# Performance work log

Measured on AMD Instinct MI355X. Metric: run time of the kernel, lower is better.

Reference implementation:

```python
import jax, jax.numpy as jnp
import numpy as np

N = 100000      # num nodes
E = 1000000     # num edges
R = 50          # num relations
B = 2           # num bases (hard-coded in source)
IN, HID, OUT = 128, 64, 64


def setup_inputs() -> dict:
    key = jax.random.key(0)
    ks = jax.random.split(key, 12)
    def xavier(k, shape):
        fan_in, fan_out = shape[-2], shape[-1]
        lim = (6.0 / (fan_in + fan_out)) ** 0.5
        return jax.random.uniform(k, shape, jnp.float32, -lim, lim)
    return {
        "node_emb": xavier(ks[0], (N, IN)),
        "basis1": xavier(ks[1], (B, IN, HID)),
        "comp1": xavier(ks[2], (R, B)),
        "loop_w1": xavier(ks[3], (IN, HID)),
        "bias1": jnp.zeros((HID,), jnp.float32),
        "basis2": xavier(ks[4], (B, HID, OUT)),
        "comp2": xavier(ks[5], (R, B)),
        "loop_w2": xavier(ks[6], (HID, OUT)),
        "bias2": jnp.zeros((OUT,), jnp.float32),
        "src": jax.random.randint(ks[7], (E,), 0, N, jnp.int32),
        "dst": jax.random.randint(ks[8], (E,), 0, N, jnp.int32),
        "etypes": jax.random.randint(ks[9], (E,), 0, R, jnp.int32),
    }


def _rel_graph_conv(h, basis, comp, loop_w, bias, src, dst, etypes, act):
    # Basis-decomposed R-GCN layer (DGL RelGraphConv, regularizer='basis'):
    #   W_r = sum_b comp[r,b] * basis[b];  m_e = W_{etype_e} h_{src_e}
    # Low-rank form: project with each basis first (2 dense GEMMs), then mix
    # per-edge with the relation coefficients, then scatter-add by dst.
    hb = jnp.einsum('nd,bdo->nbo', h, basis)          # [N, B, out]
    c = comp[etypes]                                   # [E, B]
    msg = jnp.einsum('eb,ebo->eo', c, hb[src])         # gather [E,B,out] -> [E,out]
    agg = jax.ops.segment_sum(msg, dst, num_segments=h.shape[0])  # scatter-add
    return act(agg + h @ loop_w + bias)                # self-loop + bias + activation


def reference(node_emb, basis1, comp1, loop_w1, bias1,
              basis2, comp2, loop_w2, bias2, src, dst, etypes):
    h = _rel_graph_conv(node_emb, basis1, comp1, loop_w1, bias1,
                        src, dst, etypes, jnp.tanh)
    out = _rel_graph_conv(h, basis2, comp2, loop_w2, bias2,
                          src, dst, etypes, jax.nn.relu)
    return out
```

## Files before the change

### kernel.cpp

```cpp
#include <hip/hip_runtime.h>
#include <math.h>


typedef short          short8 __attribute__((ext_vector_type(8)));
typedef float          f32x4  __attribute__((ext_vector_type(4)));
typedef unsigned short u16;

#define NCHUNK 256

static __device__ __forceinline__ u16 bf16_rne(float x) {
    unsigned u = __float_as_uint(x);
    return (u16)((u + 0x7fffu + ((u >> 16) & 1u)) >> 16);
}
static __device__ __forceinline__ float bf16_f32(u16 h) {
    return __uint_as_float(((unsigned)h) << 16);
}

#define DOT2_ACC(acc, vv, cc) \
    asm("v_dot2_f32_bf16 %0, %1, %2, %0" : "+v"(acc) : "v"(vv), "s"(cc))

__device__ __forceinline__ void wconv_body(
    int tid,
    const float* __restrict__ loopw1, const float* __restrict__ basis1,
    const float* __restrict__ loopw2, const float* __restrict__ basis2,
    const float* __restrict__ comp1, const float* __restrict__ comp2,
    u16* __restrict__ wt1h, u16* __restrict__ wt1l,
    u16* __restrict__ wt2h, u16* __restrict__ wt2l,
    unsigned* __restrict__ cpk1, unsigned* __restrict__ cpk2)
{
    if (tid < 192 * 128) {
        const int j = tid >> 7, k = tid & 127;
        const float w = (j < 64)
            ? loopw1[k * 64 + j]
            : basis1[(size_t)((j - 64) >> 6) * (128 * 64) + k * 64 + ((j - 64) & 63)];
        const u16 h = bf16_rne(w);
        wt1h[tid] = h;
        wt1l[tid] = bf16_rne(w - bf16_f32(h));
    }
    if (tid < 192 * 64) {
        const int j = tid >> 6, k = tid & 63;
        const float w = (j < 64)
            ? loopw2[k * 64 + j]
            : basis2[(size_t)((j - 64) >> 6) * (64 * 64) + k * 64 + ((j - 64) & 63)];
        const u16 h = bf16_rne(w);
        wt2h[tid] = h;
        wt2l[tid] = bf16_rne(w - bf16_f32(h));
    }
    if (tid < 50) {
        cpk1[tid] = (unsigned)bf16_rne(comp1[2 * tid])
                  | ((unsigned)bf16_rne(comp1[2 * tid + 1]) << 16);
        cpk2[tid] = (unsigned)bf16_rne(comp2[2 * tid])
                  | ((unsigned)bf16_rne(comp2[2 * tid + 1]) << 16);
    }
}

__global__ __launch_bounds__(256) void prep_count(
    const int* __restrict__ dst, int* __restrict__ cnt, int nE, int nB,
    const float* __restrict__ loopw1, const float* __restrict__ basis1,
    const float* __restrict__ loopw2, const float* __restrict__ basis2,
    const float* __restrict__ comp1, const float* __restrict__ comp2,
    u16* __restrict__ wt1h, u16* __restrict__ wt1l,
    u16* __restrict__ wt2h, u16* __restrict__ wt2l,
    unsigned* __restrict__ cpk1, unsigned* __restrict__ cpk2)
{
    const int t = threadIdx.x;
    if (blockIdx.x >= NCHUNK) {
        wconv_body((blockIdx.x - NCHUNK) * 256 + t,
                   loopw1, basis1, loopw2, basis2, comp1, comp2,
                   wt1h, wt1l, wt2h, wt2l, cpk1, cpk2);
        return;
    }
    __shared__ int lh[1024];
    for (int b = t; b < 1024; b += 256) lh[b] = 0;
    __syncthreads();
    const int chunk = (nE + NCHUNK - 1) / NCHUNK;
    const int e0 = blockIdx.x * chunk;
    const int e1 = min(nE, e0 + chunk);
    for (int e = e0 + t; e < e1; e += 256)
        atomicAdd(&lh[dst[e] >> 7], 1);
    __syncthreads();
    for (int b = t; b < nB; b += 256)
        cnt[blockIdx.x * nB + b] = lh[b];
}

template<int K>
__global__ __launch_bounds__(512, 2) void rgcn_dense_mfma(
    const float* __restrict__ x,
    const u16* __restrict__ wth,
    const u16* __restrict__ wtl,
    const float* __restrict__ bias,
    float* __restrict__ self,
    unsigned* __restrict__ hbb,
    int nNodes)
{
    constexpr int KC    = K / 32;
    constexpr int GW    = K / 8;
    constexpr int GMW   = GW - 1;
    constexpr int CCOLS = (K == 128) ? 48 : 192;
    constexpr int NCH   = 192 / CCOLS;
    constexpr int JH    = CCOLS / 16;
    constexpr int TG    = CCOLS * 2 * GW;
    constexpr int PG    = TG / 512;
    constexpr int BUF   = CCOLS * 2 * K;
    __shared__ u16 wlds[24576];

    const int n0   = blockIdx.x * 128;
    const int lane = threadIdx.x & 63;
    const int w    = threadIdx.x >> 6;
    const int rl   = lane & 15;
    const int kb   = lane >> 4;

    const int row = n0 + w * 16 + rl;
    short8 Ah[KC], Al[KC];
    #pragma unroll
    for (int kc = 0; kc < KC; ++kc) {
        float v[8];
        if (row < nNodes) {
            const float* xp = x + (size_t)row * K + kc * 32 + kb * 8;
            const float4 a = *reinterpret_cast<const float4*>(xp);
            const float4 b = *reinterpret_cast<const float4*>(xp + 4);
            v[0] = a.x; v[1] = a.y; v[2] = a.z; v[3] = a.w;
            v[4] = b.x; v[5] = b.y; v[6] = b.z; v[7] = b.w;
        } else {
            #pragma unroll
            for (int i = 0; i < 8; ++i) v[i] = 0.f;
        }
        #pragma unroll
        for (int i = 0; i < 8; ++i) {
            const u16 h = bf16_rne(v[i]);
            Ah[kc][i] = (short)h;
            Al[kc][i] = (short)bf16_rne(v[i] - bf16_f32(h));
        }
    }

    f32x4 acc[12];
    #pragma unroll
    for (int j = 0; j < 12; ++j) acc[j] = (f32x4){0.f, 0.f, 0.f, 0.f};

    auto load_chunk = [&](int cc, short8* sreg) {
        #pragma unroll
        for (int i = 0; i < PG; ++i) {
            const int gi = (int)threadIdx.x + i * 512;
            const int ch = gi / (2 * GW);
            const int r2 = gi - ch * 2 * GW;
            const int s  = r2 / GW;
            const int g  = r2 - s * GW;
            sreg[i] = *reinterpret_cast<const short8*>(
                (s == 0 ? wth : wtl) + (size_t)(cc * CCOLS + ch) * K + g * 8);
        }
    };
    auto write_chunk = [&](u16* buf, const short8* sreg) {
        #pragma unroll
        for (int i = 0; i < PG; ++i) {
            const int gi = (int)threadIdx.x + i * 512;
            const int ch = gi / (2 * GW);
            const int r2 = gi - ch * 2 * GW;
            const int s  = r2 / GW;
            const int g  = r2 - s * GW;
            *reinterpret_cast<short8*>(
                &buf[((ch * 2 + s) * GW + (g ^ (ch & GMW))) * 8]) = sreg[i];
        }
    };
    auto compute = [&](int cc, const u16* buf) {
        #pragma unroll
        for (int j16h = 0; j16h < JH; ++j16h) {
            const int ch = j16h * 16 + rl;
            const u16* bbase = &buf[(ch * 2) * GW * 8];
            #pragma unroll
            for (int kc = 0; kc < KC; ++kc) {
                const int gp = (kc * 4 + kb) ^ (ch & GMW);
                const short8 Bh =
                    *reinterpret_cast<const short8*>(bbase + gp * 8);
                const short8 Bl =
                    *reinterpret_cast<const short8*>(bbase + (GW + gp) * 8);
                f32x4 a = acc[cc * JH + j16h];
                a = __builtin_amdgcn_mfma_f32_16x16x32_bf16(Ah[kc], Bh, a, 0, 0, 0);
                a = __builtin_amdgcn_mfma_f32_16x16x32_bf16(Ah[kc], Bl, a, 0, 0, 0);
                a = __builtin_amdgcn_mfma_f32_16x16x32_bf16(Al[kc], Bh, a, 0, 0, 0);
                acc[cc * JH + j16h] = a;
            }
        }
    };

    if constexpr (NCH == 1) {
        short8 s0[PG];
        load_chunk(0, s0);
        write_chunk(wlds, s0);
        __syncthreads();
        compute(0, wlds);
    } else {
        short8 s0[PG];
        load_chunk(0, s0);
        write_chunk(wlds, s0);
        __syncthreads();
        #pragma unroll
        for (int cc = 0; cc < 4; ++cc) {
            short8 sn[PG];
            if (cc < 3) load_chunk(cc + 1, sn);
            compute(cc, &wlds[(cc & 1) * BUF]);
            __syncthreads();
            if (cc < 3) {
                write_chunk(&wlds[((cc + 1) & 1) * BUF], sn);
                __syncthreads();
            }
        }
    }

    const int rowbase = n0 + w * 16 + kb * 4;
    #pragma unroll
    for (int j16 = 0; j16 < 4; ++j16) {
        const float bj = bias[j16 * 16 + rl];
        #pragma unroll
        for (int r = 0; r < 4; ++r) {
            const int rr = rowbase + r;
            if (rr < nNodes)
                self[(size_t)rr * 64 + j16 * 16 + rl] = acc[j16][r] + bj;
        }
    }
    #pragma unroll
    for (int j16 = 4; j16 < 8; ++j16) {
        #pragma unroll
        for (int r = 0; r < 4; ++r) {
            const int rr = rowbase + r;
            if (rr < nNodes)
                hbb[(size_t)rr * 64 + (j16 - 4) * 16 + rl] =
                    (unsigned)bf16_rne(acc[j16][r])
                  | ((unsigned)bf16_rne(acc[j16 + 4][r]) << 16);
        }
    }
}

__global__ __launch_bounds__(NCHUNK) void bkt_chunkscan(
    int* __restrict__ cnt, int* __restrict__ tot, int nB)
{
    __shared__ int sm[NCHUNK];
    const int b = blockIdx.x, t = threadIdx.x;
    const int v = cnt[t * nB + b];
    sm[t] = v;
    __syncthreads();
    for (int off = 1; off < NCHUNK; off <<= 1) {
        const int u = (t >= off) ? sm[t - off] : 0;
        __syncthreads();
        sm[t] += u;
        __syncthreads();
    }
    cnt[t * nB + b] = sm[t] - v;
    if (t == NCHUNK - 1) tot[b] = sm[t];
}

__global__ __launch_bounds__(1024) void bkt_boff(
    const int* __restrict__ tot, int* __restrict__ boff, int nB, int nE)
{
    __shared__ int sm[1024];
    const int t = threadIdx.x;
    const int v = (t < nB) ? tot[t] : 0;
    sm[t] = v; __syncthreads();
    for (int off = 1; off < 1024; off <<= 1) {
        const int u = (t >= off) ? sm[t - off] : 0;
        __syncthreads();
        sm[t] += u;
        __syncthreads();
    }
    if (t < nB) boff[t] = sm[t] - v;
    if (t == 0) boff[nB] = nE;
}

__global__ __launch_bounds__(256) void bkt_scatter(
    const int* __restrict__ src, const int* __restrict__ dst,
    const int* __restrict__ et, const int* __restrict__ cnt,
    const int* __restrict__ boff, unsigned* __restrict__ rec,
    int nE, int nB)
{
    __shared__ int lcur[1024];
    const int t = threadIdx.x;
    const int c = blockIdx.x;
    for (int b = t; b < nB; b += 256)
        lcur[b] = boff[b] + cnt[c * nB + b];
    __syncthreads();
    const int chunk = (nE + NCHUNK - 1) / NCHUNK;
    const int e0 = c * chunk;
    const int e1 = min(nE, e0 + chunk);
    for (int e = e0 + t; e < e1; e += 256) {
        const int d = dst[e];
        const int p = atomicAdd(&lcur[d >> 7], 1);
        rec[p] = ((unsigned)(d & 127) << 23)
               | ((unsigned)src[e] << 6)
               | (unsigned)et[e];
    }
}

__global__ __launch_bounds__(256) void bkt_sort(
    const unsigned* __restrict__ rec, unsigned* __restrict__ rec2,
    const int* __restrict__ boff, int* __restrict__ rowptr,
    int nNodes)
{
    __shared__ int cnt[128];
    __shared__ int pos[128];
    const int b = blockIdx.x;
    const int t = threadIdx.x;
    const int beg = boff[b], end = boff[b + 1];
    if (t < 128) cnt[t] = 0;
    __syncthreads();
    for (int i = beg + t; i < end; i += 256)
        atomicAdd(&cnt[rec[i] >> 23], 1);
    __syncthreads();
    if (t < 128) pos[t] = cnt[t];
    __syncthreads();
    for (int off = 1; off < 128; off <<= 1) {
        int u = 0;
        if (t < 128 && t >= off) u = pos[t - off];
        __syncthreads();
        if (t < 128) pos[t] += u;
        __syncthreads();
    }
    if (t < 128) {
        const int ex = beg + pos[t] - cnt[t];
        pos[t] = ex;
        const int n = (b << 7) + t;
        if (n < nNodes) rowptr[n] = ex;
    }
    __syncthreads();
    for (int i = beg + t; i < end; i += 256) {
        const unsigned r = rec[i];
        const int p = atomicAdd(&pos[r >> 23], 1);
        rec2[p] = r;
    }
}

template<int ACT>
__global__ __launch_bounds__(256) void rgcn_agg(
    const unsigned* __restrict__ hbb,
    const unsigned* __restrict__ cpk,
    const int* __restrict__ rowptr,
    const unsigned* __restrict__ rec2,
    float* __restrict__ io,
    int nNodes, int nEdges)
{
    const int lane = threadIdx.x & 63;
    const int w  = (blockIdx.x * 256 + threadIdx.x) >> 6;
    const int nW = (gridDim.x * 256) >> 6;
    for (int n = w; n < nNodes; n += nW) {
        const int beg = rowptr[n];
        const int end = (n == nNodes - 1) ? nEdges : rowptr[n + 1];
        const float self = io[(size_t)n * 64 + lane];
        float acc0 = 0.f, acc1 = 0.f;
        for (int base = beg; base < end; base += 64) {
            const int cnt = min(64, end - base);
            const unsigned r = (lane < cnt) ? rec2[base + lane] : 0u;
            int i = 0;
            for (; i + 8 <= cnt; i += 8) {
                int ss[8]; unsigned cp[8];
                #pragma unroll
                for (int k = 0; k < 8; ++k) {
                    const unsigned rk =
                        (unsigned)__builtin_amdgcn_readlane((int)r, i + k);
                    ss[k] = (int)((rk >> 6) & 0x1FFFFu);
                    cp[k] = cpk[rk & 63u];
                }
                unsigned v[8];
                #pragma unroll
                for (int k = 0; k < 8; ++k)
                    v[k] = hbb[(size_t)ss[k] * 64 + lane];
                #pragma unroll
                for (int k = 0; k < 8; ++k) {
                    if (k & 1) { DOT2_ACC(acc1, v[k], cp[k]); }
                    else       { DOT2_ACC(acc0, v[k], cp[k]); }
                }
            }
            for (; i + 2 <= cnt; i += 2) {
                const unsigned rA =
                    (unsigned)__builtin_amdgcn_readlane((int)r, i);
                const unsigned rB =
                    (unsigned)__builtin_amdgcn_readlane((int)r, i + 1);
                const unsigned cA = cpk[rA & 63u], cB = cpk[rB & 63u];
                const unsigned vA = hbb[(size_t)((rA >> 6) & 0x1FFFFu) * 64 + lane];
                const unsigned vB = hbb[(size_t)((rB >> 6) & 0x1FFFFu) * 64 + lane];
                DOT2_ACC(acc0, vA, cA);
                DOT2_ACC(acc1, vB, cB);
            }
            if (i < cnt) {
                const unsigned rA =
                    (unsigned)__builtin_amdgcn_readlane((int)r, i);
                const unsigned cA = cpk[rA & 63u];
                const unsigned vA = hbb[(size_t)((rA >> 6) & 0x1FFFFu) * 64 + lane];
                DOT2_ACC(acc0, vA, cA);
            }
        }
        float o = self + acc0 + acc1;
        o = (ACT == 0) ? tanhf(o) : fmaxf(o, 0.f);
        io[(size_t)n * 64 + lane] = o;
    }
}

extern "C" void kernel_launch(void* const* d_in, const int* in_sizes, int n_in,
                              void* d_out, int out_size, void* d_ws, size_t ws_size,
                              hipStream_t stream)
{
    const float* node_emb = (const float*)d_in[0];
    const float* basis1   = (const float*)d_in[1];
    const float* comp1    = (const float*)d_in[2];
    const float* loop_w1  = (const float*)d_in[3];
    const float* bias1    = (const float*)d_in[4];
    const float* basis2   = (const float*)d_in[5];
    const float* comp2    = (const float*)d_in[6];
    const float* loop_w2  = (const float*)d_in[7];
    const float* bias2    = (const float*)d_in[8];
    const int*   src      = (const int*)d_in[9];
    const int*   dst      = (const int*)d_in[10];
    const int*   et       = (const int*)d_in[11];

    const int N = in_sizes[0] / 128;
    const int E = in_sizes[9];
    const int nB = (N + 127) / 128;

    float* out = (float*)d_out;

    unsigned* hbb    = (unsigned*)d_ws;
    float*    h      = (float*)(hbb + (size_t)N * 64);
    unsigned* rec    = (unsigned*)(h + (size_t)N * 64);
    unsigned* rec2   = rec + E;
    int*      cnt    = (int*)(rec2 + E);
    int*      tot    = cnt + NCHUNK * nB;
    int*      boff   = tot + nB;
    int*      rowptr = boff + nB + 1;
    u16*      wt1h   = (u16*)(rowptr + N);
    u16*      wt1l   = wt1h + 192 * 128;
    u16*      wt2h   = wt1l + 192 * 128;
    u16*      wt2l   = wt2h + 192 * 64;
    unsigned* cpk1   = (unsigned*)(wt2l + 192 * 64);
    unsigned* cpk2   = cpk1 + 64;

    const int nBlkDense = (N + 127) / 128;
    const int nBlkAgg   = (N + 3) / 4;

    prep_count<<<NCHUNK + 96, 256, 0, stream>>>(
        dst, cnt, E, nB, loop_w1, basis1, loop_w2, basis2, comp1, comp2,
        wt1h, wt1l, wt2h, wt2l, cpk1, cpk2);

    bkt_chunkscan<<<nB, NCHUNK, 0, stream>>>(cnt, tot, nB);
    bkt_boff     <<<1,    1024, 0, stream>>>(tot, boff, nB, E);
    bkt_scatter  <<<NCHUNK, 256, 0, stream>>>(src, dst, et, cnt, boff, rec, E, nB);
    bkt_sort     <<<nB,     256, 0, stream>>>(rec, rec2, boff, rowptr, N);

    rgcn_dense_mfma<128><<<nBlkDense, 512, 0, stream>>>(
        node_emb, wt1h, wt1l, bias1, h, hbb, N);
    rgcn_agg<0><<<nBlkAgg, 256, 0, stream>>>(
        hbb, cpk1, rowptr, rec2, h, N, E);

    rgcn_dense_mfma<64><<<nBlkDense, 512, 0, stream>>>(
        h, wt2h, wt2l, bias2, out, hbb, N);
    rgcn_agg<1><<<nBlkAgg, 256, 0, stream>>>(
        hbb, cpk2, rowptr, rec2, out, N, E);
}
```

Baseline: 191.0 us.

## Make dense MFMA kernel persistent with resident weights and prefetched A tiles

The dense projection kernel now loads the full 192-column split-bf16 weight matrix into LDS once per block and loops persistently over 128-row node tiles. A fixed grid of 256 or 512 blocks replaces one block per tile. Each iteration prefetches the next tile's activations into registers while the current tile computes. This removes the repeated per-tile weight staging and the chunked double-buffering syncs. In exchange it uses more LDS (96KB for K=128), which may cut occupancy to one block per CU, and adds register pressure from the prefetch buffers.

```diff
diff --git a/kernel.cpp b/kernel.cpp
--- a/kernel.cpp
+++ b/kernel.cpp
@@ -93,79 +93,70 @@
     unsigned* __restrict__ hbb,
     int nNodes)
 {
-    constexpr int KC    = K / 32;
-    constexpr int GW    = K / 8;
-    constexpr int GMW   = GW - 1;
-    constexpr int CCOLS = (K == 128) ? 48 : 192;
-    constexpr int NCH   = 192 / CCOLS;
-    constexpr int JH    = CCOLS / 16;
-    constexpr int TG    = CCOLS * 2 * GW;
-    constexpr int PG    = TG / 512;
-    constexpr int BUF   = CCOLS * 2 * K;
-    __shared__ u16 wlds[24576];
-
-    const int n0   = blockIdx.x * 128;
+    constexpr int KC  = K / 32;
+    constexpr int GW  = K / 8;
+    constexpr int GMW = GW - 1;
+    __shared__ u16 wlds[192 * 2 * K];
+
     const int lane = threadIdx.x & 63;
     const int w    = threadIdx.x >> 6;
     const int rl   = lane & 15;
     const int kb   = lane >> 4;
 
-    const int row = n0 + w * 16 + rl;
-    short8 Ah[KC], Al[KC];
-    #pragma unroll
-    for (int kc = 0; kc < KC; ++kc) {
-        float v[8];
-        if (row < nNodes) {
-            const float* xp = x + (size_t)row * K + kc * 32 + kb * 8;
-            const float4 a = *reinterpret_cast<const float4*>(xp);
-            const float4 b = *reinterpret_cast<const float4*>(xp + 4);
-            v[0] = a.x; v[1] = a.y; v[2] = a.z; v[3] = a.w;
-            v[4] = b.x; v[5] = b.y; v[6] = b.z; v[7] = b.w;
-        } else {
+    for (int gi = threadIdx.x; gi < 192 * 2 * GW; gi += 512) {
+        const int ch = gi / (2 * GW);
+        const int r2 = gi - ch * 2 * GW;
+        const int s  = r2 / GW;
+        const int g  = r2 - s * GW;
+        const short8 vv = *reinterpret_cast<const short8*>(
+            (s == 0 ? wth : wtl) + (size_t)ch * K + g * 8);
+        *reinterpret_cast<short8*>(
+            &wlds[((ch * 2 + s) * GW + (g ^ (ch & GMW))) * 8]) = vv;
+    }
+    __syncthreads();
+
+    const int nT = (nNodes + 127) >> 7;
+
+    auto loadA = [&](int tile, short8* AhD, short8* AlD) {
+        const int row = (tile << 7) + w * 16 + rl;
+        #pragma unroll
+        for (int kc = 0; kc < KC; ++kc) {
+            float v[8];
+            if (row < nNodes) {
+                const float* xp = x + (size_t)row * K + kc * 32 + kb * 8;
+                const float4 a = *reinterpret_cast<const float4*>(xp);
+                const float4 b = *reinterpret_cast<const float4*>(xp + 4);
+                v[0] = a.x; v[1] = a.y; v[2] = a.z; v[3] = a.w;
+                v[4] = b.x; v[5] = b.y; v[6] = b.z; v[7] = b.w;
+            } else {
+                #pragma unroll
+                for (int i = 0; i < 8; ++i) v[i] = 0.f;
+            }
             #pragma unroll
-            for (int i = 0; i < 8; ++i) v[i] = 0.f;
-        }
+            for (int i = 0; i < 8; ++i) {
+                const u16 h = bf16_rne(v[i]);
+                AhD[kc][i] = (short)h;
+                AlD[kc][i] = (short)bf16_rne(v[i] - bf16_f32(h));
+            }
+        }
+    };
+
+    short8 Ah[KC], Al[KC], Ph[KC], Pl[KC];
+    int tile = blockIdx.x;
+    if (tile < nT) loadA(tile, Ah, Al);
+
+    for (; tile < nT; tile += gridDim.x) {
+        const int nxt = tile + gridDim.x;
+        if (nxt < nT) loadA(nxt, Ph, Pl);
+
+        f32x4 acc[12];
         #pragma unroll
-        for (int i = 0; i < 8; ++i) {
-            const u16 h = bf16_rne(v[i]);
-            Ah[kc][i] = (short)h;
-            Al[kc][i] = (short)bf16_rne(v[i] - bf16_f32(h));
-        }
-    }
-
-    f32x4 acc[12];
-    #pragma unroll
-    for (int j = 0; j < 12; ++j) acc[j] = (f32x4){0.f, 0.f, 0.f, 0.f};
-
-    auto load_chunk = [&](int cc, short8* sreg) {
+        for (int j = 0; j < 12; ++j) acc[j] = (f32x4){0.f, 0.f, 0.f, 0.f};
+
         #pragma unroll
-        for (int i = 0; i < PG; ++i) {
-            const int gi = (int)threadIdx.x + i * 512;
-            const int ch = gi / (2 * GW);
-            const int r2 = gi - ch * 2 * GW;
-            const int s  = r2 / GW;
-            const int g  = r2 - s * GW;
-            sreg[i] = *reinterpret_cast<const short8*>(
-                (s == 0 ? wth : wtl) + (size_t)(cc * CCOLS + ch) * K + g * 8);
-        }
-    };
-    auto write_chunk = [&](u16* buf, const short8* sreg) {
-        #pragma unroll
-        for (int i = 0; i < PG; ++i) {
-            const int gi = (int)threadIdx.x + i * 512;
-            const int ch = gi / (2 * GW);
-            const int r2 = gi - ch * 2 * GW;
-            const int s  = r2 / GW;
-            const int g  = r2 - s * GW;
-            *reinterpret_cast<short8*>(
-                &buf[((ch * 2 + s) * GW + (g ^ (ch & GMW))) * 8]) = sreg[i];
-        }
-    };
-    auto compute = [&](int cc, const u16* buf) {
-        #pragma unroll
-        for (int j16h = 0; j16h < JH; ++j16h) {
+        for (int j16h = 0; j16h < 12; ++j16h) {
             const int ch = j16h * 16 + rl;
-            const u16* bbase = &buf[(ch * 2) * GW * 8];
+            const u16* bbase = &wlds[(ch * 2) * GW * 8];
             #pragma unroll
             for (int kc = 0; kc < KC; ++kc) {
                 const int gp = (kc * 4 + kb) ^ (ch & GMW);
@@ -173,59 +164,40 @@
                     *reinterpret_cast<const short8*>(bbase + gp * 8);
                 const short8 Bl =
                     *reinterpret_cast<const short8*>(bbase + (GW + gp) * 8);
-                f32x4 a = acc[cc * JH + j16h];
+                f32x4 a = acc[j16h];
                 a = __builtin_amdgcn_mfma_f32_16x16x32_bf16(Ah[kc], Bh, a, 0, 0, 0);
                 a = __builtin_amdgcn_mfma_f32_16x16x32_bf16(Ah[kc], Bl, a, 0, 0, 0);
                 a = __builtin_amdgcn_mfma_f32_16x16x32_bf16(Al[kc], Bh, a, 0, 0, 0);
-                acc[cc * JH + j16h] = a;
-            }
-        }
-    };
-
-    if constexpr (NCH == 1) {
-        short8 s0[PG];
-        load_chunk(0, s0);
-        write_chunk(wlds, s0);
-        __syncthreads();
-        compute(0, wlds);
-    } else {
-        short8 s0[PG];
-        load_chunk(0, s0);
-        write_chunk(wlds, s0);
-        __syncthreads();
+                acc[j16h] = a;
+            }
+        }
+
+        const int rowbase = (tile << 7) + w * 16 + kb * 4;
         #pragma unroll
-        for (int cc = 0; cc < 4; ++cc) {
-            short8 sn[PG];
-            if (cc < 3) load_chunk(cc + 1, sn);
-            compute(cc, &wlds[(cc & 1) * BUF]);
-            __syncthreads();
-            if (cc < 3) {
-                write_chunk(&wlds[((cc + 1) & 1) * BUF], sn);
-                __syncthreads();
-            }
-        }
-    }
-
-    const int rowbase = n0 + w * 16 + kb * 4;
-    #pragma unroll
-    for (int j16 = 0; j16 < 4; ++j16) {
-        const float bj = bias[j16 * 16 + rl];
+        for (int j16 = 0; j16 < 4; ++j16) {
+            const float bj = bias[j16 * 16 + rl];
+            #pragma unroll
+            for (int r = 0; r < 4; ++r) {
+                const int rr = rowbase + r;
+                if (rr < nNodes)
+                    self[(size_t)rr * 64 + j16 * 16 + rl] = acc[j16][r] + bj;
+            }
+        }
         #pragma unroll
-        for (int r = 0; r < 4; ++r) {
-            const int rr = rowbase + r;
-            if (rr < nNodes)
-                self[(size_t)rr * 64 + j16 * 16 + rl] = acc[j16][r] + bj;
-        }
-    }
-    #pragma unroll
-    for (int j16 = 4; j16 < 8; ++j16) {
-        #pragma unroll
-        for (int r = 0; r < 4; ++r) {
-            const int rr = rowbase + r;
-            if (rr < nNodes)
-                hbb[(size_t)rr * 64 + (j16 - 4) * 16 + rl] =
-                    (unsigned)bf16_rne(acc[j16][r])
-                  | ((unsigned)bf16_rne(acc[j16 + 4][r]) << 16);
+        for (int j16 = 4; j16 < 8; ++j16) {
+            #pragma unroll
+            for (int r = 0; r < 4; ++r) {
+                const int rr = rowbase + r;
+                if (rr < nNodes)
+                    hbb[(size_t)rr * 64 + (j16 - 4) * 16 + rl] =
+                        (unsigned)bf16_rne(acc[j16][r])
+                      | ((unsigned)bf16_rne(acc[j16 + 4][r]) << 16);
+            }
+        }
+
+        if (nxt < nT) {
+            #pragma unroll
+            for (int kc = 0; kc < KC; ++kc) { Ah[kc] = Ph[kc]; Al[kc] = Pl[kc]; }
         }
     }
 }
@@ -430,8 +402,7 @@
     unsigned* cpk1   = (unsigned*)(wt2l + 192 * 64);
     unsigned* cpk2   = cpk1 + 64;
 
-    const int nBlkDense = (N + 127) / 128;
-    const int nBlkAgg   = (N + 3) / 4;
+    const int nBlkAgg = (N + 3) / 4;
 
     prep_count<<<NCHUNK + 96, 256, 0, stream>>>(
         dst, cnt, E, nB, loop_w1, basis1, loop_w2, basis2, comp1, comp2,
@@ -442,12 +413,12 @@
     bkt_scatter  <<<NCHUNK, 256, 0, stream>>>(src, dst, et, cnt, boff, rec, E, nB);
     bkt_sort     <<<nB,     256, 0, stream>>>(rec, rec2, boff, rowptr, N);
 
-    rgcn_dense_mfma<128><<<nBlkDense, 512, 0, stream>>>(
+    rgcn_dense_mfma<128><<<256, 512, 0, stream>>>(
         node_emb, wt1h, wt1l, bias1, h, hbb, N);
     rgcn_agg<0><<<nBlkAgg, 256, 0, stream>>>(
         hbb, cpk1, rowptr, rec2, h, N, E);
 
-    rgcn_dense_mfma<64><<<nBlkDense, 512, 0, stream>>>(
+    rgcn_dense_mfma<64><<<512, 512, 0, stream>>>(
         h, wt2h, wt2l, bias2, out, hbb, N);
     rgcn_agg<1><<<nBlkAgg, 256, 0, stream>>>(
         hbb, cpk2, rowptr, rec2, out, N, E);
```

Measured after the change: 332.1 us. 1.74x slower.
